# Performance work log

Hardware: AMD Instinct MI355X
Metric: run time of the kernel (lower is better)

The kernel has to match this reference:

```python
import jax, jax.numpy as jnp
import numpy as np

N, C, H, W = 8, 19, 512, 512


def setup_inputs() -> dict:
    key = jax.random.key(0)
    k1, k2 = jax.random.split(key)
    logits = jax.random.normal(k1, (N, C, H, W), dtype=jnp.float32)
    labels = jax.random.randint(k2, (N, H, W), 0, C, dtype=jnp.int32)
    return {"logits": logits, "labels": labels}


def reference(logits, labels):
    # softmax over class dim, then flatten to [P, C] (P = N*H*W)
    num_classes = logits.shape[1]
    probas = jax.nn.softmax(logits, axis=1)
    probas = jnp.moveaxis(probas, 1, -1).reshape(-1, num_classes)  # [P, C]
    labels_flat = labels.reshape(-1)  # [P]

    # fg[p, c] = 1 if labels[p] == c (ground truth, detached)
    fg = jax.nn.one_hot(labels_flat, num_classes, dtype=probas.dtype)  # [P, C]

    errors = jnp.abs(fg - probas)  # [P, C]
    # per-class descending sort of errors (vectorized over all classes)
    perm = jnp.argsort(-errors, axis=0)  # [P, C]
    errors_sorted = jnp.take_along_axis(errors, perm, axis=0)
    fg_sorted = jnp.take_along_axis(fg, perm, axis=0)

    # Lovasz gradient (Alg. 1), per class column
    gts = jnp.sum(fg_sorted, axis=0)  # [C]
    intersection = gts - jnp.cumsum(fg_sorted, axis=0)  # [P, C]
    union = gts + jnp.cumsum(1.0 - fg_sorted, axis=0)  # [P, C]
    jaccard = 1.0 - intersection / union
    grad = jnp.concatenate([jaccard[:1], jaccard[1:] - jaccard[:-1]], axis=0)

    losses = jnp.sum(errors_sorted * grad, axis=0)  # [C]
    return jnp.mean(losses)
```

## Files before the change

### kernel.cpp

```cpp
#include <hip/hip_runtime.h>

#define CLS   19
#define NBINS 128
#define HWSZ  (512 * 512)
#define NPIX  (8 * HWSZ)
#define HIST  (CLS * NBINS)
#define CSTR  (HIST + 16)
#define NC    2
#define NSUB  8
#define TPB   256

__global__ __launch_bounds__(TPB)
void lovasz_hist(const float* __restrict__ logits, const int* __restrict__ labels,
                 unsigned* __restrict__ blk_hist, float* __restrict__ out, int gpb) {
    __shared__ unsigned h[NC * CSTR];
    const int tid = threadIdx.x;
    for (int i = tid; i < NC * CSTR; i += TPB) h[i] = 0u;
    if (blockIdx.x == 0 && tid == 0) out[0] = 0.f;
    __syncthreads();

    const unsigned copy = (unsigned)tid & (NC - 1);
    const int base_g = blockIdx.x * gpb;
    for (int it = 0; it < gpb; it += TPB) {
        const int g  = base_g + it + tid;
        const int p  = g << 2;
        const int n  = p >> 18;
        const int hw = p & (HWSZ - 1);
        const float4* bp = (const float4*)(logits + (size_t)n * CLS * HWSZ + hw);

        float4 va[CLS];
#pragma unroll
        for (int c = 0; c < CLS; ++c)
            va[c] = bp[c * (HWSZ / 4)];

        float4 s = {0.f, 0.f, 0.f, 0.f};
#pragma unroll
        for (int c = 0; c < CLS; ++c) {
            va[c].x = __expf(va[c].x); s.x += va[c].x;
            va[c].y = __expf(va[c].y); s.y += va[c].y;
            va[c].z = __expf(va[c].z); s.z += va[c].z;
            va[c].w = __expf(va[c].w); s.w += va[c].w;
        }
        const float4 inv = {1.f / s.x, 1.f / s.y, 1.f / s.z, 1.f / s.w};
        const int4 lab = *(const int4*)(labels + p);

        unsigned* hc = &h[copy * CSTR];
#pragma unroll
        for (int c = 0; c < CLS; ++c) {
            float e; unsigned ic; int b;
            e = va[c].x * inv.x; ic = 1u;
            if (c == lab.x) { e = 1.f - e; ic = 0x10001u; }
            b = (int)(e * (float)NBINS); b = b > (NBINS - 1) ? (NBINS - 1) : b;
            atomicAdd(&hc[c * NBINS + b], ic);
            e = va[c].y * inv.y; ic = 1u;
            if (c == lab.y) { e = 1.f - e; ic = 0x10001u; }
            b = (int)(e * (float)NBINS); b = b > (NBINS - 1) ? (NBINS - 1) : b;
            atomicAdd(&hc[c * NBINS + b], ic);
            e = va[c].z * inv.z; ic = 1u;
            if (c == lab.z) { e = 1.f - e; ic = 0x10001u; }
            b = (int)(e * (float)NBINS); b = b > (NBINS - 1) ? (NBINS - 1) : b;
            atomicAdd(&hc[c * NBINS + b], ic);
            e = va[c].w * inv.w; ic = 1u;
            if (c == lab.w) { e = 1.f - e; ic = 0x10001u; }
            b = (int)(e * (float)NBINS); b = b > (NBINS - 1) ? (NBINS - 1) : b;
            atomicAdd(&hc[c * NBINS + b], ic);
        }
    }
    __syncthreads();
    unsigned* dst = blk_hist + (size_t)blockIdx.x * HIST;
    for (int i = tid; i < HIST; i += TPB)
        dst[i] = h[i] + h[CSTR + i];
}

__global__ __launch_bounds__(NBINS)
void lovasz_reduce(const unsigned* __restrict__ blk_hist,
                   unsigned* __restrict__ pc, unsigned* __restrict__ pf, int nblk) {
    const int c = blockIdx.x, sub = blockIdx.y, t = threadIdx.x;
    const int per = nblk / NSUB;
    unsigned cnt = 0, fg = 0;
    for (int b = sub * per; b < (sub + 1) * per; ++b) {
        const unsigned v = blk_hist[(size_t)b * HIST + c * NBINS + t];
        cnt += v & 0xFFFFu;
        fg  += v >> 16;
    }
    pc[(sub * CLS + c) * NBINS + t] = cnt;
    pf[(sub * CLS + c) * NBINS + t] = fg;
}

__global__ __launch_bounds__(NBINS)
void lovasz_final(const unsigned* __restrict__ pc, const unsigned* __restrict__ pf,
                  float* __restrict__ out) {
    __shared__ unsigned scnt[NBINS], sfg[NBINS];
    __shared__ float part[NBINS / 64];
    const int c = blockIdx.x, t = threadIdx.x;

    unsigned cnt = 0, fg = 0;
    for (int s = 0; s < NSUB; ++s) {
        cnt += pc[(s * CLS + c) * NBINS + t];
        fg  += pf[(s * CLS + c) * NBINS + t];
    }
    scnt[t] = cnt; sfg[t] = fg;
    __syncthreads();

    unsigned nb = 0, fb = 0, g = 0;
    for (int b = t + 1; b < NBINS; ++b) { nb += scnt[b]; fb += sfg[b]; }
    for (int b = 0; b < NBINS; ++b) g += sfg[b];

    const float gts = (float)g;
    const float nB = (float)nb,          fB = (float)fb;
    const float nA = nB + (float)cnt,    fA = fB + (float)fg;
    const float dB = gts + nB - fB;
    const float jB = dB > 0.f ? 1.f - (gts - fB) / dB : 0.f;
    const float dA = gts + nA - fA;
    const float jA = dA > 0.f ? 1.f - (gts - fA) / dA : 0.f;
    float contrib = (((float)t + 0.5f) * (1.f / NBINS)) * (jA - jB);

    for (int off = 32; off > 0; off >>= 1) contrib += __shfl_down(contrib, off);
    if ((t & 63) == 0) part[t >> 6] = contrib;
    __syncthreads();
    if (t == 0) {
        float loss_c = 0.f;
        for (int w = 0; w < NBINS / 64; ++w) loss_c += part[w];
        atomicAdd(out, loss_c * (1.f / (float)CLS));
    }
}

extern "C" void kernel_launch(void* const* d_in, const int* in_sizes, int n_in,
                              void* d_out, int out_size, void* d_ws, size_t ws_size,
                              hipStream_t stream) {
    const float* logits = (const float*)d_in[0];
    const int*   labels = (const int*)d_in[1];
    float*       out    = (float*)d_out;

    int nblk = 1024;
    size_t need = (size_t)nblk * HIST * 4 + 2 * (size_t)NSUB * HIST * 4;
    if (ws_size < need) nblk = 128;

    unsigned* blk_hist = (unsigned*)d_ws;
    unsigned* pc = blk_hist + (size_t)nblk * HIST;
    unsigned* pf = pc + (size_t)NSUB * HIST;

    const int gpb = (NPIX / 4) / nblk;
    lovasz_hist<<<nblk, TPB, 0, stream>>>(logits, labels, blk_hist, out, gpb);
    lovasz_reduce<<<dim3(CLS, NSUB), NBINS, 0, stream>>>(blk_hist, pc, pf, nblk);
    lovasz_final<<<CLS, NBINS, 0, stream>>>(pc, pf, out);
}
```

Measured before the change: 253.5 us.

## Merge histogram reduce and final kernels; use nontemporal loads for inputs

The two-stage cross-block histogram reduction (reduce kernel plus final kernel through global partial buffers) becomes a single final kernel. Each block handles one class with 1024 threads split into 8 chunks over source blocks, and the chunks are combined in shared memory. This removes one launch and the global round trip for the partial sums. Input logits and labels are now read with nontemporal loads to avoid polluting the cache. The trade-off is that only 19 blocks do the reduction, so per-block serial work grows.

```diff
diff --git a/kernel.cpp b/kernel.cpp
--- a/kernel.cpp
+++ b/kernel.cpp
@@ -7,8 +7,11 @@
 #define HIST  (CLS * NBINS)
 #define CSTR  (HIST + 16)
 #define NC    2
-#define NSUB  8
 #define TPB   256
+#define NCHUNK 8
+
+typedef float vf4 __attribute__((ext_vector_type(4)));
+typedef int   vi4 __attribute__((ext_vector_type(4)));
 
 __global__ __launch_bounds__(TPB)
 void lovasz_hist(const float* __restrict__ logits, const int* __restrict__ labels,
@@ -26,14 +29,14 @@
         const int p  = g << 2;
         const int n  = p >> 18;
         const int hw = p & (HWSZ - 1);
-        const float4* bp = (const float4*)(logits + (size_t)n * CLS * HWSZ + hw);
+        const vf4* bp = (const vf4*)(logits + (size_t)n * CLS * HWSZ + hw);
 
-        float4 va[CLS];
+        vf4 va[CLS];
 #pragma unroll
         for (int c = 0; c < CLS; ++c)
-            va[c] = bp[c * (HWSZ / 4)];
+            va[c] = __builtin_nontemporal_load(&bp[c * (HWSZ / 4)]);
 
-        float4 s = {0.f, 0.f, 0.f, 0.f};
+        vf4 s = {0.f, 0.f, 0.f, 0.f};
 #pragma unroll
         for (int c = 0; c < CLS; ++c) {
             va[c].x = __expf(va[c].x); s.x += va[c].x;
@@ -41,8 +44,8 @@
             va[c].z = __expf(va[c].z); s.z += va[c].z;
             va[c].w = __expf(va[c].w); s.w += va[c].w;
         }
-        const float4 inv = {1.f / s.x, 1.f / s.y, 1.f / s.z, 1.f / s.w};
-        const int4 lab = *(const int4*)(labels + p);
+        const vf4 inv = {1.f / s.x, 1.f / s.y, 1.f / s.z, 1.f / s.w};
+        const vi4 lab = __builtin_nontemporal_load((const vi4*)(labels + p));
 
         unsigned* hc = &h[copy * CSTR];
 #pragma unroll
@@ -72,57 +75,51 @@
         dst[i] = h[i] + h[CSTR + i];
 }
 
-__global__ __launch_bounds__(NBINS)
-void lovasz_reduce(const unsigned* __restrict__ blk_hist,
-                   unsigned* __restrict__ pc, unsigned* __restrict__ pf, int nblk) {
-    const int c = blockIdx.x, sub = blockIdx.y, t = threadIdx.x;
-    const int per = nblk / NSUB;
+__global__ __launch_bounds__(NCHUNK * NBINS)
+void lovasz_final(const unsigned* __restrict__ blk_hist, float* __restrict__ out,
+                  int nblk) {
+    __shared__ unsigned scnt[NCHUNK * NBINS], sfg[NCHUNK * NBINS];
+    __shared__ float part[2];
+    const int c = blockIdx.x, t = threadIdx.x;
+    const int bin = t & (NBINS - 1), chunk = t >> 7;
+    const int per = nblk / NCHUNK;
+
     unsigned cnt = 0, fg = 0;
-    for (int b = sub * per; b < (sub + 1) * per; ++b) {
-        const unsigned v = blk_hist[(size_t)b * HIST + c * NBINS + t];
+    for (int b = chunk * per; b < (chunk + 1) * per; ++b) {
+        const unsigned v = blk_hist[(size_t)b * HIST + c * NBINS + bin];
         cnt += v & 0xFFFFu;
         fg  += v >> 16;
-    }
-    pc[(sub * CLS + c) * NBINS + t] = cnt;
-    pf[(sub * CLS + c) * NBINS + t] = fg;
-}
-
-__global__ __launch_bounds__(NBINS)
-void lovasz_final(const unsigned* __restrict__ pc, const unsigned* __restrict__ pf,
-                  float* __restrict__ out) {
-    __shared__ unsigned scnt[NBINS], sfg[NBINS];
-    __shared__ float part[NBINS / 64];
-    const int c = blockIdx.x, t = threadIdx.x;
-
-    unsigned cnt = 0, fg = 0;
-    for (int s = 0; s < NSUB; ++s) {
-        cnt += pc[(s * CLS + c) * NBINS + t];
-        fg  += pf[(s * CLS + c) * NBINS + t];
     }
     scnt[t] = cnt; sfg[t] = fg;
     __syncthreads();
 
-    unsigned nb = 0, fb = 0, g = 0;
-    for (int b = t + 1; b < NBINS; ++b) { nb += scnt[b]; fb += sfg[b]; }
-    for (int b = 0; b < NBINS; ++b) g += sfg[b];
+    if (t < NBINS) {
+        unsigned tc = 0, tf = 0;
+#pragma unroll
+        for (int k = 0; k < NCHUNK; ++k) { tc += scnt[k * NBINS + t]; tf += sfg[k * NBINS + t]; }
+        scnt[t] = tc; sfg[t] = tf;
+    }
+    __syncthreads();
 
-    const float gts = (float)g;
-    const float nB = (float)nb,          fB = (float)fb;
-    const float nA = nB + (float)cnt,    fA = fB + (float)fg;
-    const float dB = gts + nB - fB;
-    const float jB = dB > 0.f ? 1.f - (gts - fB) / dB : 0.f;
-    const float dA = gts + nA - fA;
-    const float jA = dA > 0.f ? 1.f - (gts - fA) / dA : 0.f;
-    float contrib = (((float)t + 0.5f) * (1.f / NBINS)) * (jA - jB);
+    if (t < NBINS) {
+        unsigned nb = 0, fb = 0, g = 0;
+        for (int b = t + 1; b < NBINS; ++b) { nb += scnt[b]; fb += sfg[b]; }
+        for (int b = 0; b < NBINS; ++b) g += sfg[b];
 
-    for (int off = 32; off > 0; off >>= 1) contrib += __shfl_down(contrib, off);
-    if ((t & 63) == 0) part[t >> 6] = contrib;
+        const float gts = (float)g;
+        const float nB = (float)nb,            fB = (float)fb;
+        const float nA = nB + (float)scnt[t],  fA = fB + (float)sfg[t];
+        const float dB = gts + nB - fB;
+        const float jB = dB > 0.f ? 1.f - (gts - fB) / dB : 0.f;
+        const float dA = gts + nA - fA;
+        const float jA = dA > 0.f ? 1.f - (gts - fA) / dA : 0.f;
+        float contrib = (((float)t + 0.5f) * (1.f / NBINS)) * (jA - jB);
+
+        for (int off = 32; off > 0; off >>= 1) contrib += __shfl_down(contrib, off);
+        if ((t & 63) == 0) part[t >> 6] = contrib;
+    }
     __syncthreads();
-    if (t == 0) {
-        float loss_c = 0.f;
-        for (int w = 0; w < NBINS / 64; ++w) loss_c += part[w];
-        atomicAdd(out, loss_c * (1.f / (float)CLS));
-    }
+    if (t == 0) atomicAdd(out, (part[0] + part[1]) * (1.f / (float)CLS));
 }
 
 extern "C" void kernel_launch(void* const* d_in, const int* in_sizes, int n_in,
@@ -133,15 +130,11 @@
     float*       out    = (float*)d_out;
 
     int nblk = 1024;
-    size_t need = (size_t)nblk * HIST * 4 + 2 * (size_t)NSUB * HIST * 4;
-    if (ws_size < need) nblk = 128;
+    if (ws_size < (size_t)nblk * HIST * 4) nblk = 128;
 
     unsigned* blk_hist = (unsigned*)d_ws;
-    unsigned* pc = blk_hist + (size_t)nblk * HIST;
-    unsigned* pf = pc + (size_t)NSUB * HIST;
+    const int gpb = (NPIX / 4) / nblk;
 
-    const int gpb = (NPIX / 4) / nblk;
     lovasz_hist<<<nblk, TPB, 0, stream>>>(logits, labels, blk_hist, out, gpb);
-    lovasz_reduce<<<dim3(CLS, NSUB), NBINS, 0, stream>>>(blk_hist, pc, pf, nblk);
-    lovasz_final<<<CLS, NBINS, 0, stream>>>(pc, pf, out);
+    lovasz_final<<<CLS, NCHUNK * NBINS, 0, stream>>>(blk_hist, out, nblk);
 }
```

Result: faster. 242.6 us (-4.3%).
